# Performance work log

Hardware: AMD Instinct MI355X
Metric: run time of the kernel (lower is better)

Reference implementation:

```python
import jax, jax.numpy as jnp
import numpy as np

PRIOR = 0.2
TEMP = 1.0
THRESHOLD = 0.5
B, L, D, H = 8, 4096, 768, 512


def setup_inputs() -> dict:
    key = jax.random.key(0)
    k1, k2, k3, k4 = jax.random.split(key, 4)
    hidden = jax.random.normal(k1, (B, L, D), jnp.float32)
    # MLP params: Linear(D,H) -> ReLU -> Linear(H,1)
    W1 = jax.random.normal(k2, (D, H), jnp.float32) / np.sqrt(D).astype(np.float32)
    b1 = jnp.zeros((H,), jnp.float32)
    W2 = jax.random.normal(k3, (H, 1), jnp.float32) / np.sqrt(H).astype(np.float32)
    b2 = jnp.zeros((1,), jnp.float32)
    # pre-sampled uniform noise for the RelaxedBernoulli logistic reparameterization
    noise_u = jax.random.uniform(k4, (B, L), jnp.float32, minval=1e-6, maxval=1.0 - 1e-6)
    return dict(hidden=hidden, W1=W1, b1=b1, W2=W2, b2=b2, noise_u=noise_u)


def reference(hidden, W1, b1, W2, b2, noise_u):
    bs, seq_len, model_dim = hidden.shape
    # boundary MLP -> per-token logits [B, L]
    h = jax.nn.relu(jnp.einsum('bld,dh->blh', hidden, W1) + b1)
    logits = (jnp.einsum('blh,ho->blo', h, W2) + b2)[..., 0]
    # RelaxedBernoulli rsample: sigmoid((logits + logistic_noise) / temp),
    # since logit(sigmoid(logits)) == logits
    logistic_noise = jnp.log(noise_u) - jnp.log1p(-noise_u)
    soft_boundaries = jax.nn.sigmoid((logits + logistic_noise) / TEMP)
    hard_bin = (soft_boundaries > THRESHOLD).astype(soft_boundaries.dtype)
    # straight-through estimator
    hard_boundaries = soft_boundaries + jax.lax.stop_gradient(hard_bin - soft_boundaries)
    # segment id of each token: number of boundaries strictly before it
    # (boundary token is the last element of its segment)
    seg = (jnp.cumsum(hard_bin, axis=1) - hard_bin).astype(jnp.int32)  # [B, L] in [0, L)
    ids = (seg + seq_len * jnp.arange(bs, dtype=jnp.int32)[:, None]).reshape(-1)
    flat = hidden.reshape(bs * seq_len, model_dim)
    seg_sum = jax.ops.segment_sum(flat, ids, num_segments=bs * seq_len)
    seg_cnt = jax.ops.segment_sum(jnp.ones((bs * seq_len,), hidden.dtype), ids,
                                  num_segments=bs * seq_len)
    # mean pooling per segment; unused segment slots stay zero (padded to L segments,
    # equivalent to the torch [S,B,D]->transpose output up to zero padding)
    pooled = (seg_sum / jnp.maximum(seg_cnt, 1.0)[:, None]).reshape(bs, seq_len, model_dim)
    # hinge loss on boundary rate: penalize |rate - (prior+0.05)| beyond margin 0.05
    ratio = jnp.mean(hard_boundaries)
    loss = jax.nn.relu(jnp.abs(ratio - (PRIOR + 0.05)) - 0.05)
    num_boundaries = jnp.sum(hard_bin)
    total_positions = jnp.asarray(bs * seq_len, jnp.float32)
    return pooled, loss, num_boundaries, total_positions
```

## Files before the change

### kernel.cpp

```cpp
#include <hip/hip_runtime.h>
#include <hip/hip_bf16.h>
#include <math.h>

typedef __attribute__((ext_vector_type(8))) short short8;
typedef __attribute__((ext_vector_type(4))) float float4v;

#define BATCH 8
#define SEQ   4096
#define DIM   768
#define HID   512
#define M_TOK (BATCH * SEQ)

static __device__ __forceinline__ short f2bf(float x) {
    unsigned int u = __float_as_uint(x);
    unsigned int r = (u + 0x7FFFu + ((u >> 16) & 1u)) >> 16;
    return (short)r;
}

__global__ __launch_bounds__(256) void prep_kernel(const float* __restrict__ W1,
                                                   short* __restrict__ W1T,
                                                   float* __restrict__ logits,
                                                   int* __restrict__ nbtot) {
    int idx = blockIdx.x * 256 + threadIdx.x;
    if (idx < DIM * HID) {
        int k = idx / HID, n = idx % HID;
        W1T[n * DIM + k] = f2bf(W1[idx]);
    }
    if (idx < M_TOK) logits[idx] = 0.f;
    if (idx == 0) *nbtot = 0;
}

__global__ __launch_bounds__(256) void mlp_kernel(const float* __restrict__ A,
                                                  const short* __restrict__ BT,
                                                  const float* __restrict__ b1,
                                                  const float* __restrict__ W2,
                                                  float* __restrict__ logits) {
    __shared__ short As[128 * 40];
    __shared__ short Bs[128 * 40];

    const int n0 = blockIdx.x * 128;
    const int m0 = blockIdx.y * 128;
    const int tid  = threadIdx.x;
    const int srow = tid >> 1;
    const int shalf = tid & 1;
    const int wave = tid >> 6, lane = tid & 63;
    const int quad = lane >> 4, r = lane & 15;
    const int waveM = (wave & 1) * 64, waveN = (wave >> 1) * 64;

    float4v acc[4][4] = {};

    const float* aRow = A + (size_t)(m0 + srow) * DIM;
    const short* bRow = BT + (size_t)(n0 + srow) * DIM;

    for (int k0 = 0; k0 < DIM; k0 += 32) {
        const float* ap = aRow + k0 + shalf * 16;
        float4v f0 = *(const float4v*)(ap + 0);
        float4v f1 = *(const float4v*)(ap + 4);
        float4v f2 = *(const float4v*)(ap + 8);
        float4v f3 = *(const float4v*)(ap + 12);
        const short* bp = bRow + k0 + shalf * 16;
        short8 g0 = *(const short8*)(bp + 0);
        short8 g1 = *(const short8*)(bp + 8);

        __syncthreads();

        short cv[16];
#pragma unroll
        for (int i = 0; i < 4; i++) {
            cv[i]      = f2bf(f0[i]);
            cv[4 + i]  = f2bf(f1[i]);
            cv[8 + i]  = f2bf(f2[i]);
            cv[12 + i] = f2bf(f3[i]);
        }
        *(short8*)(&As[srow * 40 + shalf * 16])     = *(short8*)&cv[0];
        *(short8*)(&As[srow * 40 + shalf * 16 + 8]) = *(short8*)&cv[8];
        *(short8*)(&Bs[srow * 40 + shalf * 16])     = g0;
        *(short8*)(&Bs[srow * 40 + shalf * 16 + 8]) = g1;

        __syncthreads();

        short8 af[4], bf[4];
#pragma unroll
        for (int i = 0; i < 4; i++) {
            af[i] = *(const short8*)(&As[(waveM + i * 16 + r) * 40 + quad * 8]);
            bf[i] = *(const short8*)(&Bs[(waveN + i * 16 + r) * 40 + quad * 8]);
        }
#pragma unroll
        for (int mi = 0; mi < 4; mi++)
#pragma unroll
            for (int ni = 0; ni < 4; ni++)
                acc[mi][ni] = __builtin_amdgcn_mfma_f32_16x16x32_bf16(
                    af[mi], bf[ni], acc[mi][ni], 0, 0, 0);
    }

    float w2v[4], b1v[4];
#pragma unroll
    for (int ni = 0; ni < 4; ni++) {
        int gc = n0 + waveN + ni * 16 + r;
        w2v[ni] = W2[gc];
        b1v[ni] = b1[gc];
    }
#pragma unroll
    for (int mi = 0; mi < 4; mi++) {
#pragma unroll
        for (int v = 0; v < 4; v++) {
            float p = 0.f;
#pragma unroll
            for (int ni = 0; ni < 4; ni++) {
                float h = acc[mi][ni][v] + b1v[ni];
                h = h > 0.f ? h : 0.f;
                p += h * w2v[ni];
            }
#pragma unroll
            for (int off = 1; off < 16; off <<= 1) p += __shfl_xor(p, off, 64);
            if (r == 0) {
                int gr = m0 + waveM + mi * 16 + quad * 4 + v;
                atomicAdd(&logits[gr], p);
            }
        }
    }
}

__global__ __launch_bounds__(1024) void boundary_kernel(const float* __restrict__ logits,
                                                        const float* __restrict__ b2p,
                                                        const float* __restrict__ noise,
                                                        int* __restrict__ starts,
                                                        int* __restrict__ nseg,
                                                        int* __restrict__ nbtot) {
    const int b = blockIdx.x, tid = threadIdx.x;
    const int base = tid * 4;
    const float b2 = b2p[0];
    int h[4], c = 0;
#pragma unroll
    for (int j = 0; j < 4; j++) {
        int l = base + j;
        float u = noise[b * SEQ + l];
        float nz = logf(u) - log1pf(-u);
        float lg = logits[b * SEQ + l] + b2 + nz;
        h[j] = (lg > 0.f) ? 1 : 0;
        c += h[j];
    }
    const int lane = tid & 63, wid = tid >> 6;
    int inc = c;
    for (int off = 1; off < 64; off <<= 1) {
        int t = __shfl_up(inc, off, 64);
        if (lane >= off) inc += t;
    }
    __shared__ int wtot[16], woff[16], extra[2];
    if (lane == 63) wtot[wid] = inc;
    if (tid == 1023) extra[0] = h[3];
    __syncthreads();
    if (tid == 0) {
        int s = 0;
        for (int i = 0; i < 16; i++) { woff[i] = s; s += wtot[i]; }
        extra[1] = s;
    }
    __syncthreads();
    int run = (inc - c) + woff[wid];
#pragma unroll
    for (int j = 0; j < 4; j++) {
        int l = base + j;
        if (h[j]) {
            run++;
            if (l < SEQ - 1) starts[b * (SEQ + 1) + run] = l + 1;
        }
    }
    if (tid == 0) {
        int total = extra[1];
        int ns = total + (extra[0] ? 0 : 1);
        starts[b * (SEQ + 1)] = 0;
        starts[b * (SEQ + 1) + ns] = SEQ;
        nseg[b] = ns;
        atomicAdd(nbtot, total);
    }
}

__global__ __launch_bounds__(64) void pool_kernel(const float* __restrict__ hidden,
                                                  const int* __restrict__ starts,
                                                  const int* __restrict__ nseg,
                                                  float* __restrict__ out) {
    const int s = blockIdx.x, b = blockIdx.y;
    const int lane = threadIdx.x;
    float* orow = out + (size_t)(b * SEQ + s) * DIM;
    const int ns = nseg[b];
    if (s >= ns) {
        float4v z = {0.f, 0.f, 0.f, 0.f};
        *(float4v*)(orow + lane * 4)         = z;
        *(float4v*)(orow + (lane + 64) * 4)  = z;
        *(float4v*)(orow + (lane + 128) * 4) = z;
        return;
    }
    const int st = starts[b * (SEQ + 1) + s];
    const int en = starts[b * (SEQ + 1) + s + 1];
    float4v a0 = {0.f, 0.f, 0.f, 0.f}, a1 = a0, a2 = a0;
    const float* hbase = hidden + (size_t)(b * SEQ) * DIM;
    for (int row = st; row < en; row++) {
        const float* hr = hbase + (size_t)row * DIM;
        a0 += *(const float4v*)(hr + lane * 4);
        a1 += *(const float4v*)(hr + (lane + 64) * 4);
        a2 += *(const float4v*)(hr + (lane + 128) * 4);
    }
    const float invc = 1.f / (float)(en - st);
    a0 *= invc; a1 *= invc; a2 *= invc;
    *(float4v*)(orow + lane * 4)         = a0;
    *(float4v*)(orow + (lane + 64) * 4)  = a1;
    *(float4v*)(orow + (lane + 128) * 4) = a2;
}

__global__ void finalize_kernel(const int* __restrict__ nbtot, float* __restrict__ tail) {
    int nb = *nbtot;
    float ratio = (float)nb / (float)M_TOK;
    float d = fabsf(ratio - 0.25f) - 0.05f;
    tail[0] = d > 0.f ? d : 0.f;
    tail[1] = (float)nb;
    tail[2] = (float)M_TOK;
}

extern "C" void kernel_launch(void* const* d_in, const int* in_sizes, int n_in,
                              void* d_out, int out_size, void* d_ws, size_t ws_size,
                              hipStream_t stream) {
    const float* hidden = (const float*)d_in[0];
    const float* W1     = (const float*)d_in[1];
    const float* b1     = (const float*)d_in[2];
    const float* W2     = (const float*)d_in[3];
    const float* b2     = (const float*)d_in[4];
    const float* noise  = (const float*)d_in[5];

    char* ws = (char*)d_ws;
    short* W1T    = (short*)(ws);
    float* logits = (float*)(ws + 786432);
    int*   starts = (int*)(ws + 917504);
    int*   nseg   = (int*)(ws + 917504 + 131104);
    int*   nbtot  = nseg + 8;
    float* out    = (float*)d_out;

    prep_kernel<<<1536, 256, 0, stream>>>(W1, W1T, logits, nbtot);
    mlp_kernel<<<dim3(4, 256), 256, 0, stream>>>(hidden, W1T, b1, W2, logits);
    boundary_kernel<<<BATCH, 1024, 0, stream>>>(logits, b2, noise, starts, nseg, nbtot);
    pool_kernel<<<dim3(SEQ, BATCH), 64, 0, stream>>>(hidden, starts, nseg, out);
    finalize_kernel<<<1, 1, 0, stream>>>(nbtot, out + (size_t)M_TOK * DIM);
}
```

Baseline: 274.9 us.

## Prefetch GEMM tiles, swizzle blocks, drop atomics, and widen pool blocks

The MLP GEMM now prefetches the next K tile into registers while the current tile is converted and computed. It also remaps block ids so that groups of M tiles share the same N tiles for L2 reuse. The fp32-to-bf16 conversion switches from round-to-nearest-even to a single perm truncation, and the per-token logit atomics become plain writes to 8 partial buffers summed in the boundary kernel. This removes the logits zeroing and atomic traffic, and pool blocks now handle 4 segments each to cut launch overhead. Truncation changes rounding slightly, which could flip threshold decisions for borderline tokens.

```diff
diff --git a/kernel.cpp b/kernel.cpp
--- a/kernel.cpp
+++ b/kernel.cpp
@@ -1,9 +1,9 @@
 #include <hip/hip_runtime.h>
-#include <hip/hip_bf16.h>
 #include <math.h>
 
 typedef __attribute__((ext_vector_type(8))) short short8;
 typedef __attribute__((ext_vector_type(4))) float float4v;
+typedef unsigned int uint;
 
 #define BATCH 8
 #define SEQ   4096
@@ -11,79 +11,89 @@
 #define HID   512
 #define M_TOK (BATCH * SEQ)
 
-static __device__ __forceinline__ short f2bf(float x) {
+static __device__ __forceinline__ short f2bf_rne(float x) {
     unsigned int u = __float_as_uint(x);
     unsigned int r = (u + 0x7FFFu + ((u >> 16) & 1u)) >> 16;
     return (short)r;
 }
+static __device__ __forceinline__ uint pack_bf2(float a, float b) {
+    return __builtin_amdgcn_perm(__float_as_uint(b), __float_as_uint(a), 0x07060302u);
+}
 
 __global__ __launch_bounds__(256) void prep_kernel(const float* __restrict__ W1,
-                                                   short* __restrict__ W1T,
-                                                   float* __restrict__ logits,
-                                                   int* __restrict__ nbtot) {
+                                                   short* __restrict__ W1T) {
     int idx = blockIdx.x * 256 + threadIdx.x;
     if (idx < DIM * HID) {
         int k = idx / HID, n = idx % HID;
-        W1T[n * DIM + k] = f2bf(W1[idx]);
-    }
-    if (idx < M_TOK) logits[idx] = 0.f;
-    if (idx == 0) *nbtot = 0;
+        W1T[n * DIM + k] = f2bf_rne(W1[idx]);
+    }
 }
 
 __global__ __launch_bounds__(256) void mlp_kernel(const float* __restrict__ A,
                                                   const short* __restrict__ BT,
                                                   const float* __restrict__ b1,
                                                   const float* __restrict__ W2,
-                                                  float* __restrict__ logits) {
+                                                  float* __restrict__ partial) {
     __shared__ short As[128 * 40];
     __shared__ short Bs[128 * 40];
 
-    const int n0 = blockIdx.x * 128;
-    const int m0 = blockIdx.y * 128;
+    const int id  = blockIdx.x;
+    const int m_t = (id & 7) + ((id >> 5) << 3);
+    const int n_t = (id >> 3) & 3;
+    const int m0 = m_t << 7, n0 = n_t << 7;
+
     const int tid  = threadIdx.x;
     const int srow = tid >> 1;
     const int shalf = tid & 1;
     const int wave = tid >> 6, lane = tid & 63;
     const int quad = lane >> 4, r = lane & 15;
-    const int waveM = (wave & 1) * 64, waveN = (wave >> 1) * 64;
+    const int waveM = (wave & 1) << 6, waveN = (wave >> 1) << 6;
 
     float4v acc[4][4] = {};
 
-    const float* aRow = A + (size_t)(m0 + srow) * DIM;
-    const short* bRow = BT + (size_t)(n0 + srow) * DIM;
-
-    for (int k0 = 0; k0 < DIM; k0 += 32) {
-        const float* ap = aRow + k0 + shalf * 16;
-        float4v f0 = *(const float4v*)(ap + 0);
-        float4v f1 = *(const float4v*)(ap + 4);
-        float4v f2 = *(const float4v*)(ap + 8);
-        float4v f3 = *(const float4v*)(ap + 12);
-        const short* bp = bRow + k0 + shalf * 16;
-        short8 g0 = *(const short8*)(bp + 0);
-        short8 g1 = *(const short8*)(bp + 8);
-
+    const float* aRow = A + (size_t)(m0 + srow) * DIM + shalf * 16;
+    const short* bRow = BT + (size_t)(n0 + srow) * DIM + shalf * 16;
+
+    const int lw = srow * 40 + shalf * 16;
+    const int la = (waveM + r) * 40 + quad * 8;
+    const int lb = (waveN + r) * 40 + quad * 8;
+
+    float4v fA[2][4];
+    short8  fB[2][2];
+#pragma unroll
+    for (int i = 0; i < 4; i++) fA[0][i] = *(const float4v*)(aRow + i * 4);
+    fB[0][0] = *(const short8*)(bRow);
+    fB[0][1] = *(const short8*)(bRow + 8);
+
+#pragma unroll
+    for (int it = 0; it < 24; ++it) {
+        const int cur = it & 1;
+        if (it + 1 < 24) {
+            const float* ap = aRow + (it + 1) * 32;
+            const short* bp = bRow + (it + 1) * 32;
+#pragma unroll
+            for (int i = 0; i < 4; i++) fA[cur ^ 1][i] = *(const float4v*)(ap + i * 4);
+            fB[cur ^ 1][0] = *(const short8*)(bp);
+            fB[cur ^ 1][1] = *(const short8*)(bp + 8);
+        }
+        uint pk[8];
+#pragma unroll
+        for (int i = 0; i < 4; i++) {
+            pk[2 * i]     = pack_bf2(fA[cur][i][0], fA[cur][i][1]);
+            pk[2 * i + 1] = pack_bf2(fA[cur][i][2], fA[cur][i][3]);
+        }
         __syncthreads();
-
-        short cv[16];
+        *(short8*)(&As[lw])     = *(short8*)&pk[0];
+        *(short8*)(&As[lw + 8]) = *(short8*)&pk[4];
+        *(short8*)(&Bs[lw])     = fB[cur][0];
+        *(short8*)(&Bs[lw + 8]) = fB[cur][1];
+        __syncthreads();
+
+        short8 af[4], bf[4];
 #pragma unroll
         for (int i = 0; i < 4; i++) {
-            cv[i]      = f2bf(f0[i]);
-            cv[4 + i]  = f2bf(f1[i]);
-            cv[8 + i]  = f2bf(f2[i]);
-            cv[12 + i] = f2bf(f3[i]);
-        }
-        *(short8*)(&As[srow * 40 + shalf * 16])     = *(short8*)&cv[0];
-        *(short8*)(&As[srow * 40 + shalf * 16 + 8]) = *(short8*)&cv[8];
-        *(short8*)(&Bs[srow * 40 + shalf * 16])     = g0;
-        *(short8*)(&Bs[srow * 40 + shalf * 16 + 8]) = g1;
-
-        __syncthreads();
-
-        short8 af[4], bf[4];
-#pragma unroll
-        for (int i = 0; i < 4; i++) {
-            af[i] = *(const short8*)(&As[(waveM + i * 16 + r) * 40 + quad * 8]);
-            bf[i] = *(const short8*)(&Bs[(waveN + i * 16 + r) * 40 + quad * 8]);
+            af[i] = *(const short8*)(&As[la + i * 16 * 40]);
+            bf[i] = *(const short8*)(&Bs[lb + i * 16 * 40]);
         }
 #pragma unroll
         for (int mi = 0; mi < 4; mi++)
@@ -100,6 +110,7 @@
         w2v[ni] = W2[gc];
         b1v[ni] = b1[gc];
     }
+    const int buf = n_t * 2 + (waveN >> 6);
 #pragma unroll
     for (int mi = 0; mi < 4; mi++) {
 #pragma unroll
@@ -115,18 +126,18 @@
             for (int off = 1; off < 16; off <<= 1) p += __shfl_xor(p, off, 64);
             if (r == 0) {
                 int gr = m0 + waveM + mi * 16 + quad * 4 + v;
-                atomicAdd(&logits[gr], p);
+                partial[(size_t)buf * M_TOK + gr] = p;
             }
         }
     }
 }
 
-__global__ __launch_bounds__(1024) void boundary_kernel(const float* __restrict__ logits,
+__global__ __launch_bounds__(1024) void boundary_kernel(const float* __restrict__ partial,
                                                         const float* __restrict__ b2p,
                                                         const float* __restrict__ noise,
                                                         int* __restrict__ starts,
                                                         int* __restrict__ nseg,
-                                                        int* __restrict__ nbtot) {
+                                                        int* __restrict__ nbcount) {
     const int b = blockIdx.x, tid = threadIdx.x;
     const int base = tid * 4;
     const float b2 = b2p[0];
@@ -136,7 +147,9 @@
         int l = base + j;
         float u = noise[b * SEQ + l];
         float nz = logf(u) - log1pf(-u);
-        float lg = logits[b * SEQ + l] + b2 + nz;
+        float lg = b2 + nz;
+#pragma unroll
+        for (int q = 0; q < 8; q++) lg += partial[(size_t)q * M_TOK + b * SEQ + l];
         h[j] = (lg > 0.f) ? 1 : 0;
         c += h[j];
     }
@@ -171,16 +184,16 @@
         starts[b * (SEQ + 1)] = 0;
         starts[b * (SEQ + 1) + ns] = SEQ;
         nseg[b] = ns;
-        atomicAdd(nbtot, total);
-    }
-}
-
-__global__ __launch_bounds__(64) void pool_kernel(const float* __restrict__ hidden,
-                                                  const int* __restrict__ starts,
-                                                  const int* __restrict__ nseg,
-                                                  float* __restrict__ out) {
-    const int s = blockIdx.x, b = blockIdx.y;
-    const int lane = threadIdx.x;
+        nbcount[b] = total;
+    }
+}
+
+__global__ __launch_bounds__(256) void pool_kernel(const float* __restrict__ hidden,
+                                                   const int* __restrict__ starts,
+                                                   const int* __restrict__ nseg,
+                                                   float* __restrict__ out) {
+    const int wid = threadIdx.x >> 6, lane = threadIdx.x & 63;
+    const int s = blockIdx.x * 4 + wid, b = blockIdx.y;
     float* orow = out + (size_t)(b * SEQ + s) * DIM;
     const int ns = nseg[b];
     if (s >= ns) {
@@ -207,8 +220,9 @@
     *(float4v*)(orow + (lane + 128) * 4) = a2;
 }
 
-__global__ void finalize_kernel(const int* __restrict__ nbtot, float* __restrict__ tail) {
-    int nb = *nbtot;
+__global__ void finalize_kernel(const int* __restrict__ nbcount, float* __restrict__ tail) {
+    int nb = 0;
+    for (int i = 0; i < BATCH; i++) nb += nbcount[i];
     float ratio = (float)nb / (float)M_TOK;
     float d = fabsf(ratio - 0.25f) - 0.05f;
     tail[0] = d > 0.f ? d : 0.f;
@@ -227,16 +241,16 @@
     const float* noise  = (const float*)d_in[5];
 
     char* ws = (char*)d_ws;
-    short* W1T    = (short*)(ws);
-    float* logits = (float*)(ws + 786432);
-    int*   starts = (int*)(ws + 917504);
-    int*   nseg   = (int*)(ws + 917504 + 131104);
-    int*   nbtot  = nseg + 8;
-    float* out    = (float*)d_out;
-
-    prep_kernel<<<1536, 256, 0, stream>>>(W1, W1T, logits, nbtot);
-    mlp_kernel<<<dim3(4, 256), 256, 0, stream>>>(hidden, W1T, b1, W2, logits);
-    boundary_kernel<<<BATCH, 1024, 0, stream>>>(logits, b2, noise, starts, nseg, nbtot);
-    pool_kernel<<<dim3(SEQ, BATCH), 64, 0, stream>>>(hidden, starts, nseg, out);
-    finalize_kernel<<<1, 1, 0, stream>>>(nbtot, out + (size_t)M_TOK * DIM);
-}
+    short* W1T     = (short*)(ws);
+    float* partial = (float*)(ws + 786432);
+    int*   starts  = (int*)(ws + 786432 + 1048576);
+    int*   nseg    = (int*)(ws + 786432 + 1048576 + 131104);
+    int*   nbcount = nseg + 8;
+    float* out     = (float*)d_out;
+
+    prep_kernel<<<1536, 256, 0, stream>>>(W1, W1T);
+    mlp_kernel<<<1024, 256, 0, stream>>>(hidden, W1T, b1, W2, partial);
+    boundary_kernel<<<BATCH, 1024, 0, stream>>>(partial, b2, noise, starts, nseg, nbcount);
+    pool_kernel<<<dim3(SEQ / 4, BATCH), 256, 0, stream>>>(hidden, starts, nseg, out);
+    finalize_kernel<<<1, 1, 0, stream>>>(nbcount, out + (size_t)M_TOK * DIM);
+}
```

New measurement: 256.2 us. -6.8%, faster.
